# Kernel optimization log

Measured on AMD Instinct MI355X. Metric: run time of the kernel, lower is better.

The kernel has to match this reference:

```python
import jax, jax.numpy as jnp
import numpy as np

B, T, D_IN, H, D_OUT = 32, 2048, 128, 256, 256


def setup_inputs() -> dict:
    key = jax.random.key(0)
    ks = jax.random.split(key, 12)
    sx = 1.0 / np.sqrt(D_IN)
    sh = 1.0 / np.sqrt(H)
    return {
        "x": jax.random.normal(ks[0], (B, T, D_IN), dtype=jnp.float32),
        "h0": jnp.zeros((B, H), dtype=jnp.float32),
        "Wz": jax.random.normal(ks[1], (D_IN, H), dtype=jnp.float32) * sx,
        "Uz": jax.random.normal(ks[2], (H, H), dtype=jnp.float32) * sh,
        "bz": jnp.zeros((H,), dtype=jnp.float32),
        "Wr": jax.random.normal(ks[3], (D_IN, H), dtype=jnp.float32) * sx,
        "Ur": jax.random.normal(ks[4], (H, H), dtype=jnp.float32) * sh,
        "br": jnp.zeros((H,), dtype=jnp.float32),
        "Wh": jax.random.normal(ks[5], (D_IN, H), dtype=jnp.float32) * sx,
        "Uh": jax.random.normal(ks[6], (H, H), dtype=jnp.float32) * sh,
        "bh": jnp.zeros((H,), dtype=jnp.float32),
        "Wo": jax.random.normal(ks[7], (H, D_OUT), dtype=jnp.float32) * sh,
        "bo": jnp.zeros((D_OUT,), dtype=jnp.float32),
    }


def reference(x, h0, Wz, Uz, bz, Wr, Ur, br, Wh, Uh, bh, Wo, bo):
    # TimeDistributed: swap [B,T,*] -> [T,B,*], loop cell over time collecting
    # every cell output per step, swap back. Here the cell is a GRU emitting
    # (y_t, h_t) with h_t also carried as the recurrent state.
    def step(h, xt):  # xt: [B, D_IN], h: [B, H]
        z = jax.nn.sigmoid(xt @ Wz + h @ Uz + bz)
        r = jax.nn.sigmoid(xt @ Wr + h @ Ur + br)
        hh = jnp.tanh(xt @ Wh + (r * h) @ Uh + bh)
        hn = (1.0 - z) * h + z * hh
        y = hn @ Wo + bo
        return hn, (y, hn)

    xT = jnp.swapaxes(x, 0, 1)  # [T, B, D_IN]
    _, (ys, hs) = jax.lax.scan(step, h0, xT)
    # stack back to batch-major: [B, T, D_OUT], [B, T, H]
    return jnp.swapaxes(ys, 0, 1), jnp.swapaxes(hs, 0, 1)
```

## Files before the change

### kernel.cpp

```cpp
#include <hip/hip_runtime.h>

#define B_   32
#define T_   2048
#define DIN  128
#define H_   256
#define DOUT 256

typedef _Float16 h2_t __attribute__((ext_vector_type(2)));

__device__ __forceinline__ float fdot2a(unsigned int a, unsigned int b, float c) {
#if defined(__has_builtin) && __has_builtin(__builtin_amdgcn_fdot2)
  return __builtin_amdgcn_fdot2(__builtin_bit_cast(h2_t, a),
                                __builtin_bit_cast(h2_t, b), c, false);
#else
  h2_t x = __builtin_bit_cast(h2_t, a), y = __builtin_bit_cast(h2_t, b);
  return c + (float)x[0] * (float)y[0] + (float)x[1] * (float)y[1];
#endif
}

__device__ __forceinline__ float dot256(const unsigned int* uc, const uint4* hp) {
  float a0 = 0.f, a1 = 0.f, a2 = 0.f, a3 = 0.f;
#pragma unroll
  for (int k8 = 0; k8 < 32; ++k8) {
    uint4 hq = hp[k8];
    a0 = fdot2a(uc[4 * k8 + 0], hq.x, a0);
    a1 = fdot2a(uc[4 * k8 + 1], hq.y, a1);
    a2 = fdot2a(uc[4 * k8 + 2], hq.z, a2);
    a3 = fdot2a(uc[4 * k8 + 3], hq.w, a3);
  }
  return (a0 + a1) + (a2 + a3);
}

__global__ __launch_bounds__(256) void k_gates(
    const float* __restrict__ x,
    const float* __restrict__ Wz, const float* __restrict__ Wr,
    const float* __restrict__ Wh,
    const float* __restrict__ bz, const float* __restrict__ br,
    const float* __restrict__ bh,
    _Float16* __restrict__ Gzr,
    _Float16* __restrict__ Gh)
{
  __shared__ __align__(16) float sx[32][DIN];
  const int gate = blockIdx.y;
  const float* W = (gate == 0) ? Wz : (gate == 1) ? Wr : Wh;
  const float* bias = (gate == 0) ? bz : (gate == 1) ? br : bh;
  const int row0 = blockIdx.x * 32;
  const int tid = threadIdx.x;

  const float4* xg = (const float4*)(x + (size_t)row0 * DIN);
  float4* sx4 = (float4*)&sx[0][0];
#pragma unroll
  for (int m = 0; m < 4; ++m) sx4[tid + 256 * m] = xg[tid + 256 * m];
  __syncthreads();

  const int j = tid;
  const float bj = bias[j];
  float acc[32];
#pragma unroll
  for (int i = 0; i < 32; ++i) acc[i] = 0.f;

#pragma unroll 2
  for (int k4 = 0; k4 < DIN / 4; ++k4) {
    float w0 = W[(size_t)(4 * k4 + 0) * H_ + j];
    float w1 = W[(size_t)(4 * k4 + 1) * H_ + j];
    float w2 = W[(size_t)(4 * k4 + 2) * H_ + j];
    float w3 = W[(size_t)(4 * k4 + 3) * H_ + j];
#pragma unroll
    for (int i = 0; i < 32; ++i) {
      float4 xv = *(const float4*)&sx[i][4 * k4];
      acc[i] = fmaf(xv.x, w0, acc[i]);
      acc[i] = fmaf(xv.y, w1, acc[i]);
      acc[i] = fmaf(xv.z, w2, acc[i]);
      acc[i] = fmaf(xv.w, w3, acc[i]);
    }
  }

  if (gate < 2) {
    _Float16* Gp = Gzr + (size_t)row0 * 512 + gate * H_ + j;
#pragma unroll
    for (int i = 0; i < 32; ++i) Gp[(size_t)i * 512] = (_Float16)(acc[i] + bj);
  } else {
    _Float16* Gp = Gh + (size_t)row0 * H_ + j;
#pragma unroll
    for (int i = 0; i < 32; ++i) Gp[(size_t)i * H_] = (_Float16)(acc[i] + bj);
  }
}

__global__ __launch_bounds__(768, 3) void k_scan(
    const float* __restrict__ h0,
    const float* __restrict__ Uz, const float* __restrict__ Ur,
    const float* __restrict__ Uh,
    const _Float16* __restrict__ Gzr, const _Float16* __restrict__ Gh,
    float* __restrict__ hs)
{
  __shared__ __align__(16) _Float16 h_h[H_];
  __shared__ __align__(16) _Float16 rh_h[H_];
  __shared__ float h_f[H_];
  __shared__ float z_s[H_];

  const int b = blockIdx.x;
  const int tid = threadIdx.x;
  const int g = tid >> 8;
  const int j = tid & 255;
  const float* U = (g == 0) ? Uz : (g == 1) ? Ur : Uh;

  unsigned int uc[128];
#pragma unroll
  for (int k2 = 0; k2 < 128; ++k2) {
    float a = U[(size_t)(2 * k2) * H_ + j];
    float c = U[(size_t)(2 * k2 + 1) * H_ + j];
    h2_t p;
    p[0] = (_Float16)a;
    p[1] = (_Float16)c;
    uc[k2] = __builtin_bit_cast(unsigned int, p);
  }

  if (tid < H_) {
    float h = h0[(size_t)b * H_ + tid];
    h_f[tid] = h;
    h_h[tid] = (_Float16)h;
  }
  __syncthreads();

  const _Float16* Gsrc;
  size_t gstride;
  if (g < 2) {
    Gsrc = Gzr + (size_t)b * T_ * 512 + tid;
    gstride = 512;
  } else {
    Gsrc = Gh + (size_t)b * T_ * H_ + j;
    gstride = 256;
  }
  _Float16 gnx = Gsrc[0];
  float* hsb = hs + (size_t)b * T_ * H_;

#pragma unroll 1
  for (int t = 0; t < T_; ++t) {
    float gv = (float)gnx;
    int tn = (t + 1 < T_) ? (t + 1) : t;
    gnx = Gsrc[(size_t)tn * gstride];

    if (tid < 512) {
      float acc = dot256(uc, (const uint4*)h_h);
      float s = 1.f / (1.f + __expf(-(gv + acc)));
      if (g == 0)
        z_s[j] = s;
      else
        rh_h[j] = (_Float16)(s * h_f[j]);
    }
    __syncthreads();

    if (tid >= 512) {
      float acc = dot256(uc, (const uint4*)rh_h);
      float xh = gv + acc;
      float e = __expf(-2.f * xh);
      float hh = 2.f / (1.f + e) - 1.f;
      float z = z_s[j];
      float h = h_f[j];
      float hn = (1.f - z) * h + z * hh;
      h_f[j] = hn;
      h_h[j] = (_Float16)hn;
      hsb[(size_t)t * H_ + j] = hn;
    }
    __syncthreads();
  }
}

__global__ __launch_bounds__(256) void k_out(
    const float* __restrict__ hs, const float* __restrict__ Wo,
    const float* __restrict__ bo, float* __restrict__ ys)
{
  __shared__ __align__(16) float sh[32][H_];
  const int row0 = blockIdx.x * 32;
  const int tid = threadIdx.x;

  const float4* hg = (const float4*)(hs + (size_t)row0 * H_);
  float4* sh4 = (float4*)&sh[0][0];
#pragma unroll
  for (int m = 0; m < 8; ++m) sh4[tid + 256 * m] = hg[tid + 256 * m];
  __syncthreads();

  const int j = tid;
  float acc[32];
#pragma unroll
  for (int i = 0; i < 32; ++i) acc[i] = 0.f;

#pragma unroll 2
  for (int k4 = 0; k4 < H_ / 4; ++k4) {
    float w0 = Wo[(size_t)(4 * k4 + 0) * DOUT + j];
    float w1 = Wo[(size_t)(4 * k4 + 1) * DOUT + j];
    float w2 = Wo[(size_t)(4 * k4 + 2) * DOUT + j];
    float w3 = Wo[(size_t)(4 * k4 + 3) * DOUT + j];
#pragma unroll
    for (int i = 0; i < 32; ++i) {
      float4 hv = *(const float4*)&sh[i][4 * k4];
      acc[i] = fmaf(hv.x, w0, acc[i]);
      acc[i] = fmaf(hv.y, w1, acc[i]);
      acc[i] = fmaf(hv.z, w2, acc[i]);
      acc[i] = fmaf(hv.w, w3, acc[i]);
    }
  }

  const float bj = bo[j];
  float* yp = ys + (size_t)row0 * DOUT + j;
#pragma unroll
  for (int i = 0; i < 32; ++i) yp[(size_t)i * DOUT] = acc[i] + bj;
}

extern "C" void kernel_launch(void* const* d_in, const int* in_sizes, int n_in,
                              void* d_out, int out_size, void* d_ws, size_t ws_size,
                              hipStream_t stream) {
  const float* x  = (const float*)d_in[0];
  const float* h0 = (const float*)d_in[1];
  const float* Wz = (const float*)d_in[2];
  const float* Uz = (const float*)d_in[3];
  const float* bz = (const float*)d_in[4];
  const float* Wr = (const float*)d_in[5];
  const float* Ur = (const float*)d_in[6];
  const float* br = (const float*)d_in[7];
  const float* Wh = (const float*)d_in[8];
  const float* Uh = (const float*)d_in[9];
  const float* bh = (const float*)d_in[10];
  const float* Wo = (const float*)d_in[11];
  const float* bo = (const float*)d_in[12];

  float* ys = (float*)d_out;
  float* hsO = ys + (size_t)B_ * T_ * DOUT;

  _Float16* Gzr = (_Float16*)d_out;
  _Float16* Gh  = (_Float16*)d_ws;

  dim3 g1((B_ * T_) / 32, 3);
  k_gates<<<g1, 256, 0, stream>>>(x, Wz, Wr, Wh, bz, br, bh, Gzr, Gh);
  k_scan<<<B_, 768, 0, stream>>>(h0, Uz, Ur, Uh, Gzr, Gh, hsO);
  k_out<<<(B_ * T_) / 32, 256, 0, stream>>>(hsO, Wo, bo, ys);
}
```

Baseline: 3.643 ms.

## Split candidate-gate matvec across both halves of a 512-thread scan block

The scan block drops from 768 to 512 threads. Each thread keeps its z or r recurrent weights plus half of the Uh column in registers. The candidate-gate dot product is split in two: each half computes a partial sum over 128 inputs, and the two partials are combined through shared memory after an extra barrier. This keeps all threads busy during the second phase instead of leaving two thirds idle, at the cost of one more __syncthreads per step and higher register pressure (192 packed weights per thread).

```diff
diff --git a/kernel.cpp b/kernel.cpp
--- a/kernel.cpp
+++ b/kernel.cpp
@@ -22,6 +22,19 @@
   float a0 = 0.f, a1 = 0.f, a2 = 0.f, a3 = 0.f;
 #pragma unroll
   for (int k8 = 0; k8 < 32; ++k8) {
+    uint4 hq = hp[k8];
+    a0 = fdot2a(uc[4 * k8 + 0], hq.x, a0);
+    a1 = fdot2a(uc[4 * k8 + 1], hq.y, a1);
+    a2 = fdot2a(uc[4 * k8 + 2], hq.z, a2);
+    a3 = fdot2a(uc[4 * k8 + 3], hq.w, a3);
+  }
+  return (a0 + a1) + (a2 + a3);
+}
+
+__device__ __forceinline__ float dot128(const unsigned int* uc, const uint4* hp) {
+  float a0 = 0.f, a1 = 0.f, a2 = 0.f, a3 = 0.f;
+#pragma unroll
+  for (int k8 = 0; k8 < 16; ++k8) {
     uint4 hq = hp[k8];
     a0 = fdot2a(uc[4 * k8 + 0], hq.x, a0);
     a1 = fdot2a(uc[4 * k8 + 1], hq.y, a1);
@@ -86,7 +99,7 @@
   }
 }
 
-__global__ __launch_bounds__(768, 3) void k_scan(
+__global__ __launch_bounds__(512, 2) void k_scan(
     const float* __restrict__ h0,
     const float* __restrict__ Uz, const float* __restrict__ Ur,
     const float* __restrict__ Uh,
@@ -97,22 +110,30 @@
   __shared__ __align__(16) _Float16 rh_h[H_];
   __shared__ float h_f[H_];
   __shared__ float z_s[H_];
+  __shared__ float ph_s[H_];
 
   const int b = blockIdx.x;
   const int tid = threadIdx.x;
-  const int g = tid >> 8;
+  const int half = tid >> 8;
   const int j = tid & 255;
-  const float* U = (g == 0) ? Uz : (g == 1) ? Ur : Uh;
-
-  unsigned int uc[128];
+
+  const float* Uzr = half ? Ur : Uz;
+  unsigned int uzr[128];
 #pragma unroll
   for (int k2 = 0; k2 < 128; ++k2) {
-    float a = U[(size_t)(2 * k2) * H_ + j];
-    float c = U[(size_t)(2 * k2 + 1) * H_ + j];
-    h2_t p;
-    p[0] = (_Float16)a;
-    p[1] = (_Float16)c;
-    uc[k2] = __builtin_bit_cast(unsigned int, p);
+    float a = Uzr[(size_t)(2 * k2) * H_ + j];
+    float c = Uzr[(size_t)(2 * k2 + 1) * H_ + j];
+    h2_t p; p[0] = (_Float16)a; p[1] = (_Float16)c;
+    uzr[k2] = __builtin_bit_cast(unsigned int, p);
+  }
+  unsigned int uh[64];
+#pragma unroll
+  for (int k2 = 0; k2 < 64; ++k2) {
+    int k = half * 128 + 2 * k2;
+    float a = Uh[(size_t)k * H_ + j];
+    float c = Uh[(size_t)(k + 1) * H_ + j];
+    h2_t p; p[0] = (_Float16)a; p[1] = (_Float16)c;
+    uh[k2] = __builtin_bit_cast(unsigned int, p);
   }
 
   if (tid < H_) {
@@ -122,45 +143,44 @@
   }
   __syncthreads();
 
-  const _Float16* Gsrc;
-  size_t gstride;
-  if (g < 2) {
-    Gsrc = Gzr + (size_t)b * T_ * 512 + tid;
-    gstride = 512;
-  } else {
-    Gsrc = Gh + (size_t)b * T_ * H_ + j;
-    gstride = 256;
-  }
-  _Float16 gnx = Gsrc[0];
+  const _Float16* Gzr_p = Gzr + (size_t)b * T_ * 512 + half * H_ + j;
+  const _Float16* Gh_p  = Gh  + (size_t)b * T_ * H_ + j;
+  _Float16 g_zr = Gzr_p[0];
+  _Float16 g_h  = (half == 0) ? Gh_p[0] : (_Float16)0.f;
+
   float* hsb = hs + (size_t)b * T_ * H_;
 
 #pragma unroll 1
   for (int t = 0; t < T_; ++t) {
-    float gv = (float)gnx;
-    int tn = (t + 1 < T_) ? (t + 1) : t;
-    gnx = Gsrc[(size_t)tn * gstride];
-
-    if (tid < 512) {
-      float acc = dot256(uc, (const uint4*)h_h);
-      float s = 1.f / (1.f + __expf(-(gv + acc)));
-      if (g == 0)
-        z_s[j] = s;
-      else
-        rh_h[j] = (_Float16)(s * h_f[j]);
+    const float gv_zr = (float)g_zr;
+    const float gv_h  = (float)g_h;
+    const int tn = (t + 1 < T_) ? (t + 1) : t;
+    g_zr = Gzr_p[(size_t)tn * 512];
+    if (half == 0) g_h = Gh_p[(size_t)tn * H_];
+
+    {
+      float acc = dot256(uzr, (const uint4*)h_h);
+      float s = 1.f / (1.f + __expf(-(gv_zr + acc)));
+      if (half == 0) z_s[j] = s;
+      else           rh_h[j] = (_Float16)(s * h_f[j]);
     }
     __syncthreads();
 
-    if (tid >= 512) {
-      float acc = dot256(uc, (const uint4*)rh_h);
-      float xh = gv + acc;
-      float e = __expf(-2.f * xh);
-      float hh = 2.f / (1.f + e) - 1.f;
-      float z = z_s[j];
-      float h = h_f[j];
-      float hn = (1.f - z) * h + z * hh;
-      h_f[j] = hn;
-      h_h[j] = (_Float16)hn;
-      hsb[(size_t)t * H_ + j] = hn;
+    {
+      float p = dot128(uh, (const uint4*)rh_h + half * 16);
+      if (half == 1) ph_s[j] = p;
+      __syncthreads();
+      if (half == 0) {
+        float xh = gv_h + p + ph_s[j];
+        float e = __expf(-2.f * xh);
+        float hh = 2.f / (1.f + e) - 1.f;
+        float z = z_s[j];
+        float h = h_f[j];
+        float hn = (1.f - z) * h + z * hh;
+        h_f[j] = hn;
+        h_h[j] = (_Float16)hn;
+        hsb[(size_t)t * H_ + j] = hn;
+      }
     }
     __syncthreads();
   }
@@ -232,6 +252,6 @@
 
   dim3 g1((B_ * T_) / 32, 3);
   k_gates<<<g1, 256, 0, stream>>>(x, Wz, Wr, Wh, bz, br, bh, Gzr, Gh);
-  k_scan<<<B_, 768, 0, stream>>>(h0, Uz, Ur, Uh, Gzr, Gh, hsO);
+  k_scan<<<B_, 512, 0, stream>>>(h0, Uz, Ur, Uh, Gzr, Gh, hsO);
   k_out<<<(B_ * T_) / 32, 256, 0, stream>>>(hsO, Wo, bo, ys);
 }
```

New measurement: 3.515 ms. 1.04x faster.

## Batch GRU recurrence across 16 sequences per block using bf16 MFMA

Applied to the files above, without the earlier changes.

The recurrent scan is restructured so each block handles 16 batch rows and computes h@U with bf16 16x16x32 MFMA instructions, replacing the per-sequence fp16 dot2 loops. U fragments are held in registers and h/r*h are staged in swizzled LDS. The gate precompute kernel is reworked to emit bf16 values already laid out in MFMA accumulator order, so the scan can prefetch them with coalesced uint2 loads. Only 2 blocks now run the 2048-step serial chain instead of 32. This lowers per-step cost, but leaves most of the GPU idle and reduces precision to bf16.

```diff
diff --git a/kernel.cpp b/kernel.cpp
--- a/kernel.cpp
+++ b/kernel.cpp
@@ -6,29 +6,21 @@
 #define H_   256
 #define DOUT 256
 
-typedef _Float16 h2_t __attribute__((ext_vector_type(2)));
-
-__device__ __forceinline__ float fdot2a(unsigned int a, unsigned int b, float c) {
-#if defined(__has_builtin) && __has_builtin(__builtin_amdgcn_fdot2)
-  return __builtin_amdgcn_fdot2(__builtin_bit_cast(h2_t, a),
-                                __builtin_bit_cast(h2_t, b), c, false);
-#else
-  h2_t x = __builtin_bit_cast(h2_t, a), y = __builtin_bit_cast(h2_t, b);
-  return c + (float)x[0] * (float)y[0] + (float)x[1] * (float)y[1];
-#endif
-}
-
-__device__ __forceinline__ float dot256(const unsigned int* uc, const uint4* hp) {
-  float a0 = 0.f, a1 = 0.f, a2 = 0.f, a3 = 0.f;
-#pragma unroll
-  for (int k8 = 0; k8 < 32; ++k8) {
-    uint4 hq = hp[k8];
-    a0 = fdot2a(uc[4 * k8 + 0], hq.x, a0);
-    a1 = fdot2a(uc[4 * k8 + 1], hq.y, a1);
-    a2 = fdot2a(uc[4 * k8 + 2], hq.z, a2);
-    a3 = fdot2a(uc[4 * k8 + 3], hq.w, a3);
-  }
-  return (a0 + a1) + (a2 + a3);
+typedef float f32x4 __attribute__((ext_vector_type(4)));
+typedef short bf16x8 __attribute__((ext_vector_type(8)));
+
+__device__ __forceinline__ unsigned short f2bf(float f) {
+  unsigned int u = __builtin_bit_cast(unsigned int, f);
+  u += 0x7FFFu + ((u >> 16) & 1u);
+  return (unsigned short)(u >> 16);
+}
+__device__ __forceinline__ float bfq(uint2 v, int q) {
+  unsigned int u = (q & 2) ? v.y : v.x;
+  u = (q & 1) ? (u & 0xFFFF0000u) : (u << 16);
+  return __builtin_bit_cast(float, u);
+}
+__device__ __forceinline__ float sigm(float x) {
+  return __builtin_amdgcn_rcpf(1.f + __expf(-x));
 }
 
 __global__ __launch_bounds__(256) void k_gates(
@@ -37,20 +29,28 @@
     const float* __restrict__ Wh,
     const float* __restrict__ bz, const float* __restrict__ br,
     const float* __restrict__ bh,
-    _Float16* __restrict__ Gzr,
-    _Float16* __restrict__ Gh)
+    uint2* __restrict__ Gzr, uint2* __restrict__ Gh)
 {
   __shared__ __align__(16) float sx[32][DIN];
   const int gate = blockIdx.y;
   const float* W = (gate == 0) ? Wz : (gate == 1) ? Wr : Wh;
   const float* bias = (gate == 0) ? bz : (gate == 1) ? br : bh;
-  const int row0 = blockIdx.x * 32;
+  const int tg = blockIdx.x & 255;
+  const int bg = blockIdx.x >> 8;
+  const int t0 = tg * 8, b0 = bg * 4;
   const int tid = threadIdx.x;
 
-  const float4* xg = (const float4*)(x + (size_t)row0 * DIN);
-  float4* sx4 = (float4*)&sx[0][0];
-#pragma unroll
-  for (int m = 0; m < 4; ++m) sx4[tid + 256 * m] = xg[tid + 256 * m];
+  {
+    const float4* x4 = (const float4*)x;
+    float4* s4 = (float4*)&sx[0][0];
+#pragma unroll
+    for (int mm = 0; mm < 4; ++mm) {
+      int idx = tid + 256 * mm;
+      int i = idx >> 5, c4 = idx & 31;
+      int Ri = (b0 + (i >> 3)) * T_ + t0 + (i & 7);
+      s4[idx] = x4[(size_t)Ri * 32 + c4];
+    }
+  }
   __syncthreads();
 
   const int j = tid;
@@ -75,93 +75,172 @@
     }
   }
 
-  if (gate < 2) {
-    _Float16* Gp = Gzr + (size_t)row0 * 512 + gate * H_ + j;
-#pragma unroll
-    for (int i = 0; i < 32; ++i) Gp[(size_t)i * 512] = (_Float16)(acc[i] + bj);
-  } else {
-    _Float16* Gp = Gh + (size_t)row0 * H_ + j;
-#pragma unroll
-    for (int i = 0; i < 32; ++i) Gp[(size_t)i * H_] = (_Float16)(acc[i] + bj);
-  }
-}
-
-__global__ __launch_bounds__(768, 3) void k_scan(
+  const int w = j >> 5, nt = (j >> 4) & 1;
+  const int l = (bg & 3) * 16 + (j & 15);
+  const int blk = bg >> 2;
+#pragma unroll
+  for (int ti = 0; ti < 8; ++ti) {
+    int t = t0 + ti;
+    unsigned int q0 = f2bf(acc[0 * 8 + ti] + bj);
+    unsigned int q1 = f2bf(acc[1 * 8 + ti] + bj);
+    unsigned int q2 = f2bf(acc[2 * 8 + ti] + bj);
+    unsigned int q3 = f2bf(acc[3 * 8 + ti] + bj);
+    uint2 v;
+    v.x = q0 | (q1 << 16);
+    v.y = q2 | (q3 << 16);
+    if (gate < 2) {
+      size_t idx = ((((size_t)t * 2 + blk) * 2 + gate) * 16 + (w * 2 + nt)) * 64 + l;
+      Gzr[idx] = v;
+    } else {
+      size_t idx = (((size_t)t * 2 + blk) * 16 + (w * 2 + nt)) * 64 + l;
+      Gh[idx] = v;
+    }
+  }
+}
+
+__global__ __launch_bounds__(512) void k_scan(
     const float* __restrict__ h0,
     const float* __restrict__ Uz, const float* __restrict__ Ur,
     const float* __restrict__ Uh,
-    const _Float16* __restrict__ Gzr, const _Float16* __restrict__ Gh,
+    const uint2* __restrict__ Gzr, const uint2* __restrict__ Gh,
     float* __restrict__ hs)
 {
-  __shared__ __align__(16) _Float16 h_h[H_];
-  __shared__ __align__(16) _Float16 rh_h[H_];
-  __shared__ float h_f[H_];
-  __shared__ float z_s[H_];
-
-  const int b = blockIdx.x;
+  __shared__ __align__(16) unsigned short h_lds[16 * 256];
+  __shared__ __align__(16) unsigned short rh_lds[16 * 256];
+
+  const int blk = blockIdx.x;
   const int tid = threadIdx.x;
-  const int g = tid >> 8;
-  const int j = tid & 255;
-  const float* U = (g == 0) ? Uz : (g == 1) ? Ur : Uh;
-
-  unsigned int uc[128];
-#pragma unroll
-  for (int k2 = 0; k2 < 128; ++k2) {
-    float a = U[(size_t)(2 * k2) * H_ + j];
-    float c = U[(size_t)(2 * k2 + 1) * H_ + j];
-    h2_t p;
-    p[0] = (_Float16)a;
-    p[1] = (_Float16)c;
-    uc[k2] = __builtin_bit_cast(unsigned int, p);
-  }
-
-  if (tid < H_) {
-    float h = h0[(size_t)b * H_ + tid];
-    h_f[tid] = h;
-    h_h[tid] = (_Float16)h;
+  const int w = tid >> 6;
+  const int l = tid & 63;
+  const int lr = l & 15;
+  const int lh = l >> 4;
+  const int m_base = lh * 4;
+
+  bf16x8 fragU[3][2][8];
+  {
+    const float* Us[3] = {Uz, Ur, Uh};
+#pragma unroll
+    for (int g = 0; g < 3; ++g) {
+#pragma unroll
+      for (int nt = 0; nt < 2; ++nt) {
+        int n = w * 32 + nt * 16 + lr;
+#pragma unroll
+        for (int kt = 0; kt < 8; ++kt) {
+          int k0 = kt * 32 + lh * 8;
+          bf16x8 f;
+#pragma unroll
+          for (int e = 0; e < 8; ++e)
+            f[e] = (short)f2bf(Us[g][(size_t)(k0 + e) * H_ + n]);
+          fragU[g][nt][kt] = f;
+        }
+      }
+    }
+  }
+
+  float hreg[2][4];
+#pragma unroll
+  for (int nt = 0; nt < 2; ++nt) {
+    int n = w * 32 + nt * 16 + lr;
+#pragma unroll
+    for (int q = 0; q < 4; ++q) {
+      int m = m_base + q;
+      float h = h0[(size_t)(blk * 16 + m) * H_ + n];
+      hreg[nt][q] = h;
+      int byteoff = m * 512 + ((((n >> 3) ^ (m & 7)) << 4)) + (n & 7) * 2;
+      h_lds[byteoff >> 1] = f2bf(h);
+    }
   }
   __syncthreads();
 
-  const _Float16* Gsrc;
-  size_t gstride;
-  if (g < 2) {
-    Gsrc = Gzr + (size_t)b * T_ * 512 + tid;
-    gstride = 512;
-  } else {
-    Gsrc = Gh + (size_t)b * T_ * H_ + j;
-    gstride = 256;
-  }
-  _Float16 gnx = Gsrc[0];
-  float* hsb = hs + (size_t)b * T_ * H_;
+  const size_t gl0 = (size_t)(w * 2 + 0) * 64 + l;
+  const size_t gl1 = (size_t)(w * 2 + 1) * 64 + l;
+  uint2 gz0, gz1, gr0, gr1, gh0, gh1;
+  {
+    size_t bzr = ((size_t)0 * 2 + blk) * 2 * 1024;
+    size_t bh = ((size_t)0 * 2 + blk) * 1024;
+    gz0 = Gzr[bzr + gl0];        gz1 = Gzr[bzr + gl1];
+    gr0 = Gzr[bzr + 1024 + gl0]; gr1 = Gzr[bzr + 1024 + gl1];
+    gh0 = Gh[bh + gl0];          gh1 = Gh[bh + gl1];
+  }
+
+  float* hsb = hs + (size_t)(blk * 16) * T_ * H_;
+  const f32x4 zero4 = {0.f, 0.f, 0.f, 0.f};
 
 #pragma unroll 1
   for (int t = 0; t < T_; ++t) {
-    float gv = (float)gnx;
-    int tn = (t + 1 < T_) ? (t + 1) : t;
-    gnx = Gsrc[(size_t)tn * gstride];
-
-    if (tid < 512) {
-      float acc = dot256(uc, (const uint4*)h_h);
-      float s = 1.f / (1.f + __expf(-(gv + acc)));
-      if (g == 0)
-        z_s[j] = s;
-      else
-        rh_h[j] = (_Float16)(s * h_f[j]);
+    uint2 ngz0, ngz1, ngr0, ngr1, ngh0, ngh1;
+    {
+      int tn = (t + 1 < T_) ? (t + 1) : t;
+      size_t bzr = ((size_t)tn * 2 + blk) * 2 * 1024;
+      size_t bh = ((size_t)tn * 2 + blk) * 1024;
+      ngz0 = Gzr[bzr + gl0];        ngz1 = Gzr[bzr + gl1];
+      ngr0 = Gzr[bzr + 1024 + gl0]; ngr1 = Gzr[bzr + 1024 + gl1];
+      ngh0 = Gh[bh + gl0];          ngh1 = Gh[bh + gl1];
+    }
+
+    f32x4 az0 = zero4, az1 = zero4, ar0 = zero4, ar1 = zero4;
+#pragma unroll
+    for (int kt = 0; kt < 8; ++kt) {
+      int c = kt * 4 + lh;
+      int aoff = (lr * 512 + ((c ^ (lr & 7)) << 4)) >> 1;
+      bf16x8 a = *(const bf16x8*)&h_lds[aoff];
+      az0 = __builtin_amdgcn_mfma_f32_16x16x32_bf16(a, fragU[0][0][kt], az0, 0, 0, 0);
+      az1 = __builtin_amdgcn_mfma_f32_16x16x32_bf16(a, fragU[0][1][kt], az1, 0, 0, 0);
+      ar0 = __builtin_amdgcn_mfma_f32_16x16x32_bf16(a, fragU[1][0][kt], ar0, 0, 0, 0);
+      ar1 = __builtin_amdgcn_mfma_f32_16x16x32_bf16(a, fragU[1][1][kt], ar1, 0, 0, 0);
+    }
+
+    float zv[2][4];
+#pragma unroll
+    for (int nt = 0; nt < 2; ++nt) {
+      int n = w * 32 + nt * 16 + lr;
+#pragma unroll
+      for (int q = 0; q < 4; ++q) {
+        float accz = nt ? az1[q] : az0[q];
+        float accr = nt ? ar1[q] : ar0[q];
+        float gzf = bfq(nt ? gz1 : gz0, q);
+        float grf = bfq(nt ? gr1 : gr0, q);
+        float zf = sigm(accz + gzf);
+        float rf = sigm(accr + grf);
+        zv[nt][q] = zf;
+        float rh = rf * hreg[nt][q];
+        int m = m_base + q;
+        int byteoff = m * 512 + (((n >> 3) ^ (m & 7)) << 4) + (n & 7) * 2;
+        rh_lds[byteoff >> 1] = f2bf(rh);
+      }
     }
     __syncthreads();
 
-    if (tid >= 512) {
-      float acc = dot256(uc, (const uint4*)rh_h);
-      float xh = gv + acc;
-      float e = __expf(-2.f * xh);
-      float hh = 2.f / (1.f + e) - 1.f;
-      float z = z_s[j];
-      float h = h_f[j];
-      float hn = (1.f - z) * h + z * hh;
-      h_f[j] = hn;
-      h_h[j] = (_Float16)hn;
-      hsb[(size_t)t * H_ + j] = hn;
-    }
+    f32x4 ah0 = zero4, ah1 = zero4;
+#pragma unroll
+    for (int kt = 0; kt < 8; ++kt) {
+      int c = kt * 4 + lh;
+      int aoff = (lr * 512 + ((c ^ (lr & 7)) << 4)) >> 1;
+      bf16x8 a = *(const bf16x8*)&rh_lds[aoff];
+      ah0 = __builtin_amdgcn_mfma_f32_16x16x32_bf16(a, fragU[2][0][kt], ah0, 0, 0, 0);
+      ah1 = __builtin_amdgcn_mfma_f32_16x16x32_bf16(a, fragU[2][1][kt], ah1, 0, 0, 0);
+    }
+
+#pragma unroll
+    for (int nt = 0; nt < 2; ++nt) {
+      int n = w * 32 + nt * 16 + lr;
+#pragma unroll
+      for (int q = 0; q < 4; ++q) {
+        float acch = nt ? ah1[q] : ah0[q];
+        float ghf = bfq(nt ? gh1 : gh0, q);
+        float xh = acch + ghf;
+        float e = __expf(-2.f * xh);
+        float hh = 2.f * __builtin_amdgcn_rcpf(1.f + e) - 1.f;
+        float h = hreg[nt][q];
+        float hn = h + zv[nt][q] * (hh - h);
+        hreg[nt][q] = hn;
+        int m = m_base + q;
+        int byteoff = m * 512 + (((n >> 3) ^ (m & 7)) << 4) + (n & 7) * 2;
+        h_lds[byteoff >> 1] = f2bf(hn);
+        hsb[((size_t)m * T_ + t) * H_ + n] = hn;
+      }
+    }
+    gz0 = ngz0; gz1 = ngz1; gr0 = ngr0; gr1 = ngr1; gh0 = ngh0; gh1 = ngh1;
     __syncthreads();
   }
 }
@@ -227,11 +306,11 @@
   float* ys = (float*)d_out;
   float* hsO = ys + (size_t)B_ * T_ * DOUT;
 
-  _Float16* Gzr = (_Float16*)d_out;
-  _Float16* Gh  = (_Float16*)d_ws;
-
-  dim3 g1((B_ * T_) / 32, 3);
+  uint2* Gzr = (uint2*)d_out;
+  uint2* Gh  = (uint2*)d_ws;
+
+  dim3 g1(2048, 3);
   k_gates<<<g1, 256, 0, stream>>>(x, Wz, Wr, Wh, bz, br, bh, Gzr, Gh);
-  k_scan<<<B_, 768, 0, stream>>>(h0, Uz, Ur, Uh, Gzr, Gh, hsO);
+  k_scan<<<2, 512, 0, stream>>>(h0, Uz, Ur, Uh, Gzr, Gh, hsO);
   k_out<<<(B_ * T_) / 32, 256, 0, stream>>>(hsO, Wo, bo, ys);
 }
```

Measured after the change: 7.555 ms. 2.07x slower.
